# Optimization experiments

Hardware: AMD Instinct MI355X
Metric: run time of the kernel (lower is better)

## Reference

```python
import jax, jax.numpy as jnp
import numpy as np

B, S, D = 4, 2048, 1024
N_HEAD = 16
D_HEAD = D // N_HEAD
WINDOW = 1024
D_FF = 4 * D
EPS = 1e-5
NEG = -1e10


def _layernorm(x, g, b):
    mu = jnp.mean(x, axis=-1, keepdims=True)
    var = jnp.mean(jnp.square(x - mu), axis=-1, keepdims=True)
    return (x - mu) * jax.lax.rsqrt(var + EPS) * g + b


def setup_inputs() -> dict:
    key = jax.random.key(0)
    ks = jax.random.split(key, 12)
    s = 1.0 / np.sqrt(D)
    x = jax.random.normal(ks[0], (B, S, D), dtype=jnp.float32)
    key_pad_mask = jax.random.bernoulli(ks[1], 0.1, (B, S))
    return {
        "x": x,
        "key_pad_mask": key_pad_mask,
        "ln1_g": jnp.ones((D,), jnp.float32),
        "ln1_b": jnp.zeros((D,), jnp.float32),
        "wq": jax.random.normal(ks[2], (D, D), jnp.float32) * s,
        "bq": jnp.zeros((D,), jnp.float32),
        "wkv": jax.random.normal(ks[3], (D, 2 * D), jnp.float32) * s,
        "bkv": jnp.zeros((2 * D,), jnp.float32),
        "ln2_g": jnp.ones((D,), jnp.float32),
        "ln2_b": jnp.zeros((D,), jnp.float32),
        "w1": jax.random.normal(ks[4], (D, D_FF), jnp.float32) * s,
        "b1": jnp.zeros((D_FF,), jnp.float32),
        "w2": jax.random.normal(ks[5], (D_FF, D), jnp.float32) * (1.0 / np.sqrt(D_FF)),
        "b2": jnp.zeros((D,), jnp.float32),
    }


def reference(x, key_pad_mask, ln1_g, ln1_b, wq, bq, wkv, bkv, ln2_g, ln2_b, w1, b1, w2, b2):
    ln1x = _layernorm(x, ln1_g, ln1_b)
    # queries over full sequence: [B, S, nh, dh]
    q = (ln1x @ wq + bq).reshape(B, S, N_HEAD, D_HEAD)
    # keys/values from the last WINDOW tokens: [B, W, 2*nh, dh]
    kv = (ln1x[:, -WINDOW:, :] @ wkv + bkv).reshape(B, WINDOW, 2 * N_HEAD, D_HEAD)
    k, v = kv[..., :N_HEAD, :], kv[..., N_HEAD:, :]
    # NOTE: original scales by sqrt(embed_dim), not sqrt(head_dim)
    scores = jnp.einsum('bqhd,bkhd->bhqk', q, k) / np.sqrt(D)
    causal = jnp.triu(jnp.ones((S, WINDOW), dtype=bool), k=1)  # faithful to original
    pad = key_pad_mask[:, None, None, -WINDOW:]
    scores = jnp.where(pad | causal[None, None], jnp.float32(NEG), scores)
    attn = jax.nn.softmax(scores, axis=-1)
    out = jnp.einsum('bhqk,bkhd->bqhd', attn, v).reshape(B, S, D)
    h = _layernorm(out, ln2_g, ln2_b)
    h = jax.nn.silu(h @ w1 + b1) @ w2 + b2
    return h + x
```

## Files before the change

### kernel.cpp

```cpp
#include <hip/hip_runtime.h>
#include <hip/hip_bf16.h>

#define BB 4
#define SS 2048
#define DD 1024
#define HH 16
#define DHH 64
#define WW 1024
#define DFF 4096
#define MM (BB*SS)
#define NEGV (-1e10f)
#define KSC 0.045084220027780106f

using f32x4 = __attribute__((ext_vector_type(4))) float;
using s16x8 = __attribute__((ext_vector_type(8))) short;
using s16x4 = __attribute__((ext_vector_type(4))) short;
using u64 = unsigned long long;

typedef const __attribute__((address_space(1))) void* gas_t;
typedef __attribute__((address_space(3))) void* las_t;

__device__ inline short f2b(float f) {
  __hip_bfloat16 h = __float2bfloat16(f);
  return __builtin_bit_cast(short, h);
}
__device__ inline float b2f(short u) {
  __hip_bfloat16 h = __builtin_bit_cast(__hip_bfloat16, u);
  return __bfloat162float(h);
}

__device__ inline void gload_lds16(const short* g, short* lds) {
  __builtin_amdgcn_global_load_lds((gas_t)g, (las_t)lds, 16, 0, 0);
}

__device__ inline f32x4 mfma16(s16x8 a, s16x8 b, f32x4 c) {
  return __builtin_amdgcn_mfma_f32_16x16x32_bf16(a, b, c, 0, 0, 0);
}

template<int IN_BF16>
__global__ __launch_bounds__(256) void ln_kernel(const void* __restrict__ inp,
                                                 const float* __restrict__ g,
                                                 const float* __restrict__ bta,
                                                 short* __restrict__ outp) {
  int row = blockIdx.x;
  int t = threadIdx.x;
  float v[4];
  if constexpr (IN_BF16) {
    s16x4 r4 = *((const s16x4*)((const short*)inp + (size_t)row*DD) + t);
    v[0]=b2f(r4[0]); v[1]=b2f(r4[1]); v[2]=b2f(r4[2]); v[3]=b2f(r4[3]);
  } else {
    f32x4 r4 = *((const f32x4*)((const float*)inp + (size_t)row*DD) + t);
    v[0]=r4[0]; v[1]=r4[1]; v[2]=r4[2]; v[3]=r4[3];
  }
  float s = v[0]+v[1]+v[2]+v[3];
  float sq = v[0]*v[0]+v[1]*v[1]+v[2]*v[2]+v[3]*v[3];
  for (int m=1;m<64;m<<=1){ s += __shfl_xor(s,m); sq += __shfl_xor(sq,m); }
  __shared__ float red[8];
  int wv = t>>6;
  if ((t&63)==0){ red[wv]=s; red[4+wv]=sq; }
  __syncthreads();
  s  = red[0]+red[1]+red[2]+red[3];
  sq = red[4]+red[5]+red[6]+red[7];
  float mean = s*(1.f/DD);
  float rstd = rsqrtf(sq*(1.f/DD) - mean*mean + 1e-5f);
  int col = t*4;
  s16x4 o;
  #pragma unroll
  for (int j=0;j<4;++j) o[j] = f2b((v[j]-mean)*rstd*g[col+j]+bta[col+j]);
  *((s16x4*)(outp + (size_t)row*DD) + t) = o;
}

__global__ __launch_bounds__(256) void transpose_cast(const float* __restrict__ in,
                                                      short* __restrict__ out,
                                                      int K, int N) {
  __shared__ float tile[32][33];
  int n0 = blockIdx.x*32, k0 = blockIdx.y*32;
  int tx = threadIdx.x & 31, ty = threadIdx.x >> 5;
  #pragma unroll
  for (int j=0;j<4;++j) tile[ty+8*j][tx] = in[(size_t)(k0+ty+8*j)*N + n0+tx];
  __syncthreads();
  #pragma unroll
  for (int j=0;j<4;++j) out[(size_t)(n0+ty+8*j)*K + k0+tx] = f2b(tile[tx][ty+8*j]);
}

__global__ void pad_bitmask(const int* __restrict__ pad, u64* __restrict__ pm) {
  int idx = threadIdx.x;
  int b_ = idx>>4, col = idx&15;
  const int* pb = pad + b_*SS + (SS-WW);
  u64 m = 0;
  for (int c=0;c<16;++c)
    for (int nf=0;nf<4;++nf)
      if (pb[c*64+nf*16+col]) m |= (1ull << (c*4+nf));
  pm[idx] = m;
}

template<int EPI>
__global__ __launch_bounds__(256) void gemm_bt(const short* __restrict__ A,
                                               const short* __restrict__ Bt,
                                               const float* __restrict__ bias,
                                               void* __restrict__ out1,
                                               void* __restrict__ out2,
                                               const float* __restrict__ resid,
                                               int N, int K, int lgx) {
  __shared__ short As[128*32], Bs[128*32];
  int tid = threadIdx.x, l = tid&63;
  int wv = tid>>6, wm = wv>>1, wn = wv&1;
  int q8 = gridDim.x >> 3;
  int wg = (blockIdx.x & 7)*q8 + (blockIdx.x >> 3);
  int bx = wg & ((1<<lgx)-1), by = wg >> lgx;
  const short* Ablk;
  if constexpr (EPI==1) {
    int b_ = (by*128)>>10;
    int w0 = (by*128)&1023;
    Ablk = A + ((size_t)b_*SS + (SS-WW) + w0)*DD;
  } else {
    Ablk = A + (size_t)by*128*K;
  }
  const short* Bblk = Bt + (size_t)bx*128*K;
  f32x4 acc[4][4];
  #pragma unroll
  for (int i=0;i<4;++i)
    #pragma unroll
    for(int j=0;j<4;++j)
      #pragma unroll
      for(int r=0;r<4;++r) acc[i][j][r]=0.f;
  int rA = l & 15;
  int cslot = (((l>>4) ^ ((l>>1)&3))*8);
  for (int kt=0; kt<K; kt+=32) {
    __syncthreads();
    #pragma unroll
    for (int p=0;p<2;++p) {
      int s = p*256 + tid;
      int srow = s>>2;
      int scs = (((s&3) ^ ((s>>3)&3))*8);
      gload_lds16(Ablk + (size_t)srow*K + kt + scs, &As[(p*256 + (tid & ~63))*8]);
      gload_lds16(Bblk + (size_t)srow*K + kt + scs, &Bs[(p*256 + (tid & ~63))*8]);
    }
    __syncthreads();
    s16x8 af[4], bfr[4];
    #pragma unroll
    for (int mf=0;mf<4;++mf) af[mf]  = *(const s16x8*)&As[(wm*64+mf*16+rA)*32 + cslot];
    #pragma unroll
    for (int nf=0;nf<4;++nf) bfr[nf] = *(const s16x8*)&Bs[(wn*64+nf*16+rA)*32 + cslot];
    #pragma unroll
    for (int mf=0;mf<4;++mf)
      #pragma unroll
      for (int nf=0;nf<4;++nf)
        acc[mf][nf] = mfma16(af[mf], bfr[nf], acc[mf][nf]);
  }
  #pragma unroll
  for (int mf=0;mf<4;++mf) {
    #pragma unroll
    for (int nf=0;nf<4;++nf) {
      #pragma unroll
      for (int r=0;r<4;++r) {
        int row = by*128 + wm*64 + mf*16 + ((l>>4)<<2) + r;
        int col = bx*128 + wn*64 + nf*16 + (l&15);
        float v = acc[mf][nf][r] + bias[col];
        if constexpr (EPI==0) {
          ((short*)out1)[(size_t)row*N + col] = f2b(v);
        } else if constexpr (EPI==1) {
          int b_ = row>>10, w_ = row&1023;
          if (col < DD) {
            int h = col>>6, dh = col&63;
            ((short*)out1)[(((size_t)(b_*HH+h))*WW + w_)*DHH + dh] = f2b(v*KSC);
          } else {
            int cc = col - DD;
            int h = cc>>6, dh = cc&63;
            ((short*)out2)[(((size_t)(b_*HH+h))*DHH + dh)*WW + w_] = f2b(v);
          }
        } else if constexpr (EPI==2) {
          float sv = v / (1.f + __expf(-v));
          ((short*)out1)[(size_t)row*N + col] = f2b(sv);
        } else {
          ((float*)out1)[(size_t)row*N + col] = v + resid[(size_t)row*N + col];
        }
      }
    }
  }
}

template<int EPI>
__global__ __launch_bounds__(512,2) void gemm256(const short* __restrict__ A,
                                                 const short* __restrict__ Bt,
                                                 const float* __restrict__ bias,
                                                 void* __restrict__ out1,
                                                 int N, int K, int lgx) {
  __shared__ short lds[32768];
  int tid = threadIdx.x, l = tid&63, wid = tid>>6;
  int wm = wid>>2, wn = wid&3;
  int q8 = gridDim.x >> 3;
  int wg = (blockIdx.x & 7)*q8 + (blockIdx.x >> 3);
  int bx = wg & ((1<<lgx)-1), by = wg >> lgx;
  const short* Ablk = A + (size_t)by*256*K;
  const short* Bblk = Bt + (size_t)bx*256*K;
  int rA = l & 15;
  int slot_s = ((l>>4) ^ ((rA>>1)&3))*8;
  int aBase = (wm*128 + rA)*32 + slot_s;
  int bBase = (wn*64  + rA)*32 + slot_s + 8192;
  int qs = (tid&3) ^ ((tid>>3)&3);
  const short* srcA = Ablk + (size_t)(tid>>2)*K + qs*8;
  const short* srcB = Bblk + (size_t)(tid>>2)*K + qs*8;
  int dst0 = (tid & ~63)*8;
  int nt = K >> 5;
  f32x4 acc[8][4];
  #pragma unroll
  for (int i=0;i<8;++i)
    #pragma unroll
    for (int j=0;j<4;++j)
      #pragma unroll
      for (int r=0;r<4;++r) acc[i][j][r]=0.f;

  auto stage = [&](int isB, int b, int t) {
    const short* s = isB ? srcB : srcA;
    short* d = &lds[b*16384 + isB*8192 + dst0];
    gload_lds16(s + t*32,                 d);
    gload_lds16(s + (size_t)128*K + t*32, d + 4096);
  };
  s16x8 af[4], bf[4];
  auto readA = [&](int b, int mg) {
    #pragma unroll
    for (int j=0;j<4;++j) af[j] = *(const s16x8*)&lds[b*16384 + aBase + (mg*4+j)*512];
  };
  auto readB = [&](int b) {
    #pragma unroll
    for (int j=0;j<4;++j) bf[j] = *(const s16x8*)&lds[b*16384 + bBase + j*512];
  };
  auto mfmas = [&](int mg) {
    __builtin_amdgcn_s_setprio(1);
    #pragma unroll
    for (int j=0;j<4;++j)
      #pragma unroll
      for (int nf=0;nf<4;++nf)
        acc[mg*4+j][nf] = mfma16(af[j], bf[nf], acc[mg*4+j][nf]);
    __builtin_amdgcn_s_setprio(0);
  };

  stage(0,0,0); stage(1,0,0); stage(1,1,1);
  asm volatile("s_waitcnt vmcnt(2)" ::: "memory");
  __builtin_amdgcn_s_barrier();

  for (int it = 0; it < (nt>>1); ++it) {
    int t0 = 2*it;
    int t2 = t0+2; if (t2 >= nt) t2 -= nt;
    int t3 = t0+3; if (t3 >= nt) t3 -= nt;
    readB(0); readA(0,0);
    stage(0,1,t0+1);
    __builtin_amdgcn_s_barrier();
    mfmas(0);
    __builtin_amdgcn_s_barrier();
    readA(0,1);
    stage(1,0,t2);
    __builtin_amdgcn_s_barrier();
    mfmas(1);
    asm volatile("s_waitcnt vmcnt(2)" ::: "memory");
    __builtin_amdgcn_s_barrier();
    readB(1); readA(1,0);
    stage(0,0,t2);
    __builtin_amdgcn_s_barrier();
    mfmas(0);
    __builtin_amdgcn_s_barrier();
    readA(1,1);
    stage(1,1,t3);
    __builtin_amdgcn_s_barrier();
    mfmas(1);
    asm volatile("s_waitcnt vmcnt(2)" ::: "memory");
    __builtin_amdgcn_s_barrier();
  }
  asm volatile("s_waitcnt vmcnt(0)" ::: "memory");

  #pragma unroll
  for (int mf=0;mf<8;++mf) {
    #pragma unroll
    for (int nf=0;nf<4;++nf) {
      #pragma unroll
      for (int r=0;r<4;++r) {
        int row = by*256 + wm*128 + mf*16 + ((l>>4)<<2) + r;
        int col = bx*256 + wn*64 + nf*16 + rA;
        float v = acc[mf][nf][r] + bias[col];
        if constexpr (EPI==2) {
          float sv = v / (1.f + __expf(-v));
          ((short*)out1)[(size_t)row*N + col] = f2b(sv);
        } else {
          ((short*)out1)[(size_t)row*N + col] = f2b(v);
        }
      }
    }
  }
}

struct KF { s16x8 v[4][2]; };

__global__ __launch_bounds__(64,2) void attn_kernel(const short* __restrict__ q,
    const short* __restrict__ kpan, const short* __restrict__ vtpan,
    const u64* __restrict__ pmarr, short* __restrict__ outp) {
  __shared__ short P[32*72];
  int l = threadIdx.x;
  int id = blockIdx.x;
  int xcd = id & 7, slot = id >> 3;
  int bh = xcd + 8*(slot >> 6);
  int u  = 63 - (slot & 63);
  int bb = bh >> 4, h = bh & 15;
  int r0 = u*32;
  const short* kbase = kpan + (size_t)bh*WW*DHH;
  const short* vbase = vtpan + (size_t)bh*DHH*WW;
  u64 pmask = pmarr[bb*16 + (l&15)];
  const s16x8 ones8 = { 0x3F80,0x3F80,0x3F80,0x3F80,0x3F80,0x3F80,0x3F80,0x3F80 };

  s16x8 aq[2][2];
  #pragma unroll
  for (int g=0;g<2;++g)
    #pragma unroll
    for (int kf=0;kf<2;++kf)
      aq[g][kf] = *(const s16x8*)(q + ((size_t)bb*SS + r0 + g*16 + (l&15))*DD
                                    + h*DHH + (l>>4)*8 + kf*32);
  f32x4 oacc[2][4];
  float mrun[2][4], lrun[2][4], scale[2][4];
  #pragma unroll
  for (int g=0;g<2;++g)
    #pragma unroll
    for (int i=0;i<4;++i) {
      #pragma unroll
      for (int r=0;r<4;++r) oacc[g][i][r]=0.f;
      mrun[g][i]=-INFINITY; lrun[g][i]=0.f;
    }
  int dchunk = u>>1;
  int nch = dchunk+1 < 16 ? dchunk+1 : 16;

  auto loadK = [&](int c, KF& d) {
    const short* kc = kbase + (size_t)c*64*DHH;
    #pragma unroll
    for (int nf=0;nf<4;++nf) {
      const short* p = kc + (size_t)(nf*16+(l&15))*DHH + ((l>>4)*8);
      d.v[nf][0] = *(const s16x8*)p;
      d.v[nf][1] = *(const s16x8*)(p+32);
    }
  };

  auto body = [&](int c, KF& kf) {
    f32x4 sc[2][4];
    #pragma unroll
    for (int g=0;g<2;++g)
      #pragma unroll
      for (int nf=0;nf<4;++nf)
        #pragma unroll
        for (int r=0;r<4;++r) sc[g][nf][r]=0.f;
    __builtin_amdgcn_s_setprio(1);
    #pragma unroll
    for (int nf=0;nf<4;++nf)
      #pragma unroll
      for (int g=0;g<2;++g) {
        sc[g][nf] = mfma16(aq[g][0], kf.v[nf][0], sc[g][nf]);
        sc[g][nf] = mfma16(aq[g][1], kf.v[nf][1], sc[g][nf]);
      }
    __builtin_amdgcn_s_setprio(0);
    unsigned nib = (unsigned)(pmask >> (c*4)) & 15u;
    float pm[2][4];
    #pragma unroll
    for (int g=0;g<2;++g)
      #pragma unroll
      for (int r=0;r<4;++r) pm[g][r] = -INFINITY;
    if (c >= dchunk) {
      #pragma unroll
      for (int nf=0;nf<4;++nf) {
        int j = c*64 + nf*16 + (l&15);
        int padj = (int)((nib>>nf)&1u);
        #pragma unroll
        for (int g=0;g<2;++g)
          #pragma unroll
          for (int r=0;r<4;++r) {
            int sq_ = r0 + g*16 + ((l>>4)<<2) + r;
            float xv = (padj || (j > sq_)) ? NEGV : sc[g][nf][r];
            sc[g][nf][r] = xv;
            pm[g][r] = fmaxf(pm[g][r], xv);
          }
      }
    } else {
      #pragma unroll
      for (int nf=0;nf<4;++nf) {
        int padj = (int)((nib>>nf)&1u);
        #pragma unroll
        for (int g=0;g<2;++g)
          #pragma unroll
          for (int r=0;r<4;++r) {
            float xv = padj ? NEGV : sc[g][nf][r];
            sc[g][nf][r] = xv;
            pm[g][r] = fmaxf(pm[g][r], xv);
          }
      }
    }
    s16x8 vf0[4], vf1[4];
    #pragma unroll
    for (int nf=0;nf<4;++nf)
      vf0[nf] = *(const s16x8*)(vbase + (size_t)(nf*16+(l&15))*WW
                                + c*64 + ((l>>4)*8));
    int need = 0;
    #pragma unroll
    for (int g=0;g<2;++g)
      #pragma unroll
      for (int r=0;r<4;++r) need |= (pm[g][r] > mrun[g][r] + 12.f) ? 1 : 0;
    #pragma unroll
    for (int g=0;g<2;++g)
      #pragma unroll
      for (int r=0;r<4;++r) scale[g][r] = 1.f;
    if (__any(need)) {
      #pragma unroll
      for (int m=1;m<16;m<<=1)
        #pragma unroll
        for (int g=0;g<2;++g)
          #pragma unroll
          for (int r=0;r<4;++r) pm[g][r] = fmaxf(pm[g][r], __shfl_xor(pm[g][r], m));
      #pragma unroll
      for (int g=0;g<2;++g)
        #pragma unroll
        for (int r=0;r<4;++r) {
          float mn = fmaxf(mrun[g][r], pm[g][r]);
          scale[g][r] = exp2f(mrun[g][r]-mn);
          mrun[g][r] = mn;
        }
      #pragma unroll
      for (int g=0;g<2;++g)
        #pragma unroll
        for (int nf=0;nf<4;++nf)
          #pragma unroll
          for (int r=0;r<4;++r) oacc[g][nf][r] *= scale[g][r];
    }
    #pragma unroll
    for (int nf=0;nf<4;++nf)
      #pragma unroll
      for (int g=0;g<2;++g)
        #pragma unroll
        for (int r=0;r<4;++r)
          sc[g][nf][r] = exp2f(sc[g][nf][r]-mrun[g][r]);
    #pragma unroll
    for (int nf=0;nf<4;++nf)
      vf1[nf] = *(const s16x8*)(vbase + (size_t)(nf*16+(l&15))*WW
                                + c*64 + 32 + ((l>>4)*8));
    #pragma unroll
    for (int g=0;g<2;++g)
      #pragma unroll
      for (int nf=0;nf<4;++nf)
        #pragma unroll
        for (int r=0;r<4;++r)
          P[(g*16+((l>>4)<<2)+r)*72 + nf*16 + (l&15)] = f2b(sc[g][nf][r]);
    f32x4 ls2[2];
    #pragma unroll
    for (int g=0;g<2;++g)
      #pragma unroll
      for (int r=0;r<4;++r) ls2[g][r]=0.f;
    __builtin_amdgcn_s_setprio(1);
    #pragma unroll
    for (int ks=0;ks<2;++ks) {
      s16x8 ap[2];
      #pragma unroll
      for (int g=0;g<2;++g) {
        ap[g] = *(const s16x8*)&P[(g*16+(l&15))*72 + ks*32 + ((l>>4)*8)];
        ls2[g] = mfma16(ap[g], ones8, ls2[g]);
      }
      #pragma unroll
      for (int nf=0;nf<4;++nf) {
        s16x8 bv = ks ? vf1[nf] : vf0[nf];
        #pragma unroll
        for (int g=0;g<2;++g)
          oacc[g][nf] = mfma16(ap[g], bv, oacc[g][nf]);
      }
    }
    __builtin_amdgcn_s_setprio(0);
    #pragma unroll
    for (int g=0;g<2;++g)
      #pragma unroll
      for (int r=0;r<4;++r) lrun[g][r] = lrun[g][r]*scale[g][r] + ls2[g][r];
  };

  KF ka, kb;
  loadK(0, ka);
  int cend = nch, c = 0, ext = 0;
  while (true) {
    if (c == cend) {
      if (ext) break;
      ext = 1;
      int dead = 0;
      #pragma unroll
      for (int g=0;g<2;++g)
        #pragma unroll
        for (int r=0;r<4;++r) dead |= (mrun[g][r] < -5e9f) ? 1 : 0;
      if (!__any(dead)) break;
      cend = 16;
      if (c >= 16) break;
    }
    if (c+1 < 16) loadK(c+1, kb);
    body(c, ka);
    ka = kb;
    ++c;
  }

  #pragma unroll
  for (int g=0;g<2;++g)
    #pragma unroll
    for (int nf=0;nf<4;++nf)
      #pragma unroll
      for (int r=0;r<4;++r) {
        int srow = r0 + g*16 + ((l>>4)<<2) + r;
        float o = oacc[g][nf][r] / lrun[g][r];
        outp[((size_t)bb*SS + srow)*DD + h*DHH + nf*16 + (l&15)] = f2b(o);
      }
}

extern "C" void kernel_launch(void* const* d_in, const int* in_sizes, int n_in,
                              void* d_out, int out_size, void* d_ws, size_t ws_size,
                              hipStream_t stream) {
  const float* x    = (const float*)d_in[0];
  const int*   pad  = (const int*)d_in[1];
  const float* ln1g = (const float*)d_in[2];
  const float* ln1b = (const float*)d_in[3];
  const float* wq   = (const float*)d_in[4];
  const float* bq   = (const float*)d_in[5];
  const float* wkv  = (const float*)d_in[6];
  const float* bkv  = (const float*)d_in[7];
  const float* ln2g = (const float*)d_in[8];
  const float* ln2b = (const float*)d_in[9];
  const float* w1   = (const float*)d_in[10];
  const float* b1   = (const float*)d_in[11];
  const float* w2   = (const float*)d_in[12];
  const float* b2   = (const float*)d_in[13];

  char* ws = (char*)d_ws;
  const size_t MB = 1024*1024;
  short* ln1x = (short*)(ws + 0);
  short* qb   = (short*)(ws + 16*MB);
  short* kpan = (short*)(ws + 32*MB);
  short* vtp  = (short*)(ws + 40*MB);
  u64*   pmar = (u64*)  (ws + 48*MB);
  short* h1   = (short*)(ws + 0);
  short* outb = (short*)(ws + 64*MB);
  short* hb   = (short*)(ws + 80*MB);
  short* wqT  = (short*)(ws + 96*MB);
  short* wkvT = (short*)(ws + 98*MB);
  short* w1T  = (short*)(ws + 102*MB);
  short* w2T  = (short*)(ws + 110*MB);

  pad_bitmask<<<1,64,0,stream>>>(pad, pmar);
  transpose_cast<<<dim3(32,32),  256,0,stream>>>(wq,  wqT,  1024, 1024);
  transpose_cast<<<dim3(64,32),  256,0,stream>>>(wkv, wkvT, 1024, 2048);
  transpose_cast<<<dim3(128,32), 256,0,stream>>>(w1,  w1T,  1024, 4096);
  transpose_cast<<<dim3(32,128), 256,0,stream>>>(w2,  w2T,  4096, 1024);
  ln_kernel<0><<<MM,256,0,stream>>>(x, ln1g, ln1b, ln1x);
  gemm_bt<0><<<512, 256,0,stream>>>(ln1x, wqT,  bq,  qb,   nullptr, nullptr, 1024, 1024, 3);
  gemm_bt<1><<<512, 256,0,stream>>>(ln1x, wkvT, bkv, kpan, vtp,     nullptr, 2048, 1024, 4);
  attn_kernel<<<4096,64,0,stream>>>(qb, kpan, vtp, pmar, outb);
  ln_kernel<1><<<MM,256,0,stream>>>(outb, ln2g, ln2b, hb);
  gemm256<2><<<512,512,0,stream>>>(hb, w1T, b1, h1, 4096, 1024, 4);
  gemm_bt<3><<<512, 256,0,stream>>>(h1, w2T, b2, d_out, nullptr, x,       1024, 4096, 3);
}
```

Before: 403.4 us.

## Replace 128x128 GEMMs with double-buffered 256x128 pipelined GEMM kernel

Removes the simple single-buffered 128x128 gemm_bt kernel. The Q, KV and W2 projections now use a new 256x128-tile, 512-thread kernel. It double-buffers LDS, issues async global-to-LDS loads for the next k-tiles while MFMAs run, and raises wave priority around the MFMA blocks. The goal is to hide memory latency and improve reuse per tile. The cost is half as many workgroups: with 256 blocks on a GPU with about 256 CUs, that leaves a single wave of blocks and less latency hiding across blocks. The gemm256 launch bounds also drop the min-blocks hint.

```diff
diff --git a/kernel.cpp b/kernel.cpp
--- a/kernel.cpp
+++ b/kernel.cpp
@@ -95,97 +95,11 @@
 }
 
 template<int EPI>
-__global__ __launch_bounds__(256) void gemm_bt(const short* __restrict__ A,
+__global__ __launch_bounds__(512) void gemm256(const short* __restrict__ A,
                                                const short* __restrict__ Bt,
                                                const float* __restrict__ bias,
                                                void* __restrict__ out1,
-                                               void* __restrict__ out2,
-                                               const float* __restrict__ resid,
                                                int N, int K, int lgx) {
-  __shared__ short As[128*32], Bs[128*32];
-  int tid = threadIdx.x, l = tid&63;
-  int wv = tid>>6, wm = wv>>1, wn = wv&1;
-  int q8 = gridDim.x >> 3;
-  int wg = (blockIdx.x & 7)*q8 + (blockIdx.x >> 3);
-  int bx = wg & ((1<<lgx)-1), by = wg >> lgx;
-  const short* Ablk;
-  if constexpr (EPI==1) {
-    int b_ = (by*128)>>10;
-    int w0 = (by*128)&1023;
-    Ablk = A + ((size_t)b_*SS + (SS-WW) + w0)*DD;
-  } else {
-    Ablk = A + (size_t)by*128*K;
-  }
-  const short* Bblk = Bt + (size_t)bx*128*K;
-  f32x4 acc[4][4];
-  #pragma unroll
-  for (int i=0;i<4;++i)
-    #pragma unroll
-    for(int j=0;j<4;++j)
-      #pragma unroll
-      for(int r=0;r<4;++r) acc[i][j][r]=0.f;
-  int rA = l & 15;
-  int cslot = (((l>>4) ^ ((l>>1)&3))*8);
-  for (int kt=0; kt<K; kt+=32) {
-    __syncthreads();
-    #pragma unroll
-    for (int p=0;p<2;++p) {
-      int s = p*256 + tid;
-      int srow = s>>2;
-      int scs = (((s&3) ^ ((s>>3)&3))*8);
-      gload_lds16(Ablk + (size_t)srow*K + kt + scs, &As[(p*256 + (tid & ~63))*8]);
-      gload_lds16(Bblk + (size_t)srow*K + kt + scs, &Bs[(p*256 + (tid & ~63))*8]);
-    }
-    __syncthreads();
-    s16x8 af[4], bfr[4];
-    #pragma unroll
-    for (int mf=0;mf<4;++mf) af[mf]  = *(const s16x8*)&As[(wm*64+mf*16+rA)*32 + cslot];
-    #pragma unroll
-    for (int nf=0;nf<4;++nf) bfr[nf] = *(const s16x8*)&Bs[(wn*64+nf*16+rA)*32 + cslot];
-    #pragma unroll
-    for (int mf=0;mf<4;++mf)
-      #pragma unroll
-      for (int nf=0;nf<4;++nf)
-        acc[mf][nf] = mfma16(af[mf], bfr[nf], acc[mf][nf]);
-  }
-  #pragma unroll
-  for (int mf=0;mf<4;++mf) {
-    #pragma unroll
-    for (int nf=0;nf<4;++nf) {
-      #pragma unroll
-      for (int r=0;r<4;++r) {
-        int row = by*128 + wm*64 + mf*16 + ((l>>4)<<2) + r;
-        int col = bx*128 + wn*64 + nf*16 + (l&15);
-        float v = acc[mf][nf][r] + bias[col];
-        if constexpr (EPI==0) {
-          ((short*)out1)[(size_t)row*N + col] = f2b(v);
-        } else if constexpr (EPI==1) {
-          int b_ = row>>10, w_ = row&1023;
-          if (col < DD) {
-            int h = col>>6, dh = col&63;
-            ((short*)out1)[(((size_t)(b_*HH+h))*WW + w_)*DHH + dh] = f2b(v*KSC);
-          } else {
-            int cc = col - DD;
-            int h = cc>>6, dh = cc&63;
-            ((short*)out2)[(((size_t)(b_*HH+h))*DHH + dh)*WW + w_] = f2b(v);
-          }
-        } else if constexpr (EPI==2) {
-          float sv = v / (1.f + __expf(-v));
-          ((short*)out1)[(size_t)row*N + col] = f2b(sv);
-        } else {
-          ((float*)out1)[(size_t)row*N + col] = v + resid[(size_t)row*N + col];
-        }
-      }
-    }
-  }
-}
-
-template<int EPI>
-__global__ __launch_bounds__(512,2) void gemm256(const short* __restrict__ A,
-                                                 const short* __restrict__ Bt,
-                                                 const float* __restrict__ bias,
-                                                 void* __restrict__ out1,
-                                                 int N, int K, int lgx) {
   __shared__ short lds[32768];
   int tid = threadIdx.x, l = tid&63, wid = tid>>6;
   int wm = wid>>2, wn = wid&3;
@@ -289,6 +203,134 @@
   }
 }
 
+template<int EPI>
+__global__ __launch_bounds__(512) void gemm256x128(const short* __restrict__ A,
+                                                   const short* __restrict__ Bt,
+                                                   const float* __restrict__ bias,
+                                                   void* __restrict__ out1,
+                                                   void* __restrict__ out2,
+                                                   const float* __restrict__ resid,
+                                                   int N, int K, int lgx) {
+  __shared__ short lds[24576];
+  int tid = threadIdx.x, l = tid&63, wid = tid>>6;
+  int wm = wid>>1, wn = wid&1;
+  int q8 = gridDim.x >> 3;
+  int wg = (blockIdx.x & 7)*q8 + (blockIdx.x >> 3);
+  int bx = wg & ((1<<lgx)-1), by = wg >> lgx;
+  const short* Ablk;
+  if constexpr (EPI==1) {
+    int b_ = (by*256)>>10, w0 = (by*256)&1023;
+    Ablk = A + ((size_t)b_*SS + (SS-WW) + w0)*DD;
+  } else {
+    Ablk = A + (size_t)by*256*K;
+  }
+  const short* Bblk = Bt + (size_t)bx*128*K;
+  int rA = l & 15;
+  int slot_s = ((l>>4) ^ ((rA>>1)&3))*8;
+  int aBase = (wm*64 + rA)*32 + slot_s;
+  int bBase = 8192 + (wn*64 + rA)*32 + slot_s;
+  int qs = (tid&3) ^ ((tid>>3)&3);
+  const short* srcA = Ablk + (size_t)(tid>>2)*K + qs*8;
+  const short* srcB = Bblk + (size_t)(tid>>2)*K + qs*8;
+  int dst0 = (tid & ~63)*8;
+  int nt = K >> 5;
+  f32x4 acc[4][4];
+  #pragma unroll
+  for (int i=0;i<4;++i)
+    #pragma unroll
+    for (int j=0;j<4;++j)
+      #pragma unroll
+      for (int r=0;r<4;++r) acc[i][j][r]=0.f;
+
+  auto stageA = [&](int b, int t) {
+    short* d = &lds[b*12288 + dst0];
+    gload_lds16(srcA + t*32,                 d);
+    gload_lds16(srcA + (size_t)128*K + t*32, d + 4096);
+  };
+  auto stageB = [&](int b, int t) {
+    gload_lds16(srcB + t*32, &lds[b*12288 + 8192 + dst0]);
+  };
+  s16x8 af[2], bf[4];
+  auto readA = [&](int b, int mg) {
+    #pragma unroll
+    for (int j=0;j<2;++j) af[j] = *(const s16x8*)&lds[b*12288 + aBase + (mg*2+j)*512];
+  };
+  auto readB = [&](int b) {
+    #pragma unroll
+    for (int j=0;j<4;++j) bf[j] = *(const s16x8*)&lds[b*12288 + bBase + j*512];
+  };
+  auto mfmas = [&](int mg) {
+    __builtin_amdgcn_s_setprio(1);
+    #pragma unroll
+    for (int j=0;j<2;++j)
+      #pragma unroll
+      for (int nf=0;nf<4;++nf)
+        acc[mg*2+j][nf] = mfma16(af[j], bf[nf], acc[mg*2+j][nf]);
+    __builtin_amdgcn_s_setprio(0);
+  };
+
+  stageA(0,0); stageB(0,0); stageB(1,1);
+  asm volatile("s_waitcnt vmcnt(1)" ::: "memory");
+  __builtin_amdgcn_s_barrier();
+
+  for (int it = 0; it < (nt>>1); ++it) {
+    int t0 = 2*it;
+    int t2 = t0+2; if (t2 >= nt) t2 -= nt;
+    int t3 = t0+3; if (t3 >= nt) t3 -= nt;
+    readB(0); readA(0,0);
+    stageA(1,t0+1);
+    __builtin_amdgcn_s_barrier();
+    mfmas(0);
+    __builtin_amdgcn_s_barrier();
+    readA(0,1);
+    stageB(0,t2);
+    __builtin_amdgcn_s_barrier();
+    mfmas(1);
+    asm volatile("s_waitcnt vmcnt(1)" ::: "memory");
+    __builtin_amdgcn_s_barrier();
+    readB(1); readA(1,0);
+    stageA(0,t2);
+    __builtin_amdgcn_s_barrier();
+    mfmas(0);
+    __builtin_amdgcn_s_barrier();
+    readA(1,1);
+    stageB(1,t3);
+    __builtin_amdgcn_s_barrier();
+    mfmas(1);
+    asm volatile("s_waitcnt vmcnt(1)" ::: "memory");
+    __builtin_amdgcn_s_barrier();
+  }
+  asm volatile("s_waitcnt vmcnt(0)" ::: "memory");
+
+  #pragma unroll
+  for (int mf=0;mf<4;++mf) {
+    #pragma unroll
+    for (int nf=0;nf<4;++nf) {
+      #pragma unroll
+      for (int r=0;r<4;++r) {
+        int row = by*256 + wm*64 + mf*16 + ((l>>4)<<2) + r;
+        int col = bx*128 + wn*64 + nf*16 + rA;
+        float v = acc[mf][nf][r] + bias[col];
+        if constexpr (EPI==0) {
+          ((short*)out1)[(size_t)row*N + col] = f2b(v);
+        } else if constexpr (EPI==1) {
+          int b_ = row>>10, w_ = row&1023;
+          if (col < DD) {
+            int h = col>>6, dh = col&63;
+            ((short*)out1)[(((size_t)(b_*HH+h))*WW + w_)*DHH + dh] = f2b(v*KSC);
+          } else {
+            int cc = col - DD;
+            int h = cc>>6, dh = cc&63;
+            ((short*)out2)[(((size_t)(b_*HH+h))*DHH + dh)*WW + w_] = f2b(v);
+          }
+        } else {
+          ((float*)out1)[(size_t)row*N + col] = v + resid[(size_t)row*N + col];
+        }
+      }
+    }
+  }
+}
+
 struct KF { s16x8 v[4][2]; };
 
 __global__ __launch_bounds__(64,2) void attn_kernel(const short* __restrict__ q,
@@ -545,10 +587,10 @@
   transpose_cast<<<dim3(128,32), 256,0,stream>>>(w1,  w1T,  1024, 4096);
   transpose_cast<<<dim3(32,128), 256,0,stream>>>(w2,  w2T,  4096, 1024);
   ln_kernel<0><<<MM,256,0,stream>>>(x, ln1g, ln1b, ln1x);
-  gemm_bt<0><<<512, 256,0,stream>>>(ln1x, wqT,  bq,  qb,   nullptr, nullptr, 1024, 1024, 3);
-  gemm_bt<1><<<512, 256,0,stream>>>(ln1x, wkvT, bkv, kpan, vtp,     nullptr, 2048, 1024, 4);
+  gemm256x128<0><<<256,512,0,stream>>>(ln1x, wqT,  bq,  qb,   nullptr, nullptr, 1024, 1024, 3);
+  gemm256x128<1><<<256,512,0,stream>>>(ln1x, wkvT, bkv, kpan, vtp,     nullptr, 2048, 1024, 4);
   attn_kernel<<<4096,64,0,stream>>>(qb, kpan, vtp, pmar, outb);
   ln_kernel<1><<<MM,256,0,stream>>>(outb, ln2g, ln2b, hb);
   gemm256<2><<<512,512,0,stream>>>(hb, w1T, b1, h1, 4096, 1024, 4);
-  gemm_bt<3><<<512, 256,0,stream>>>(h1, w2T, b2, d_out, nullptr, x,       1024, 4096, 3);
-}
+  gemm256x128<3><<<256,512,0,stream>>>(h1, w2T, b2, d_out, nullptr, x, 1024, 4096, 3);
+}
```

Result: faster. 366.1 us (-9.3%).
